# Performance work log

Hardware: AMD Instinct MI355X
Metric: run time of the kernel (lower is better)

## Reference

```python
import jax, jax.numpy as jnp
import numpy as np

D_MODEL = 768
N_HEAD = 12

def setup_inputs() -> dict:
    key = jax.random.key(0)
    ks = jax.random.split(key, 5)
    B, T, C = 2, 2048, D_MODEL
    s = 1.0 / np.sqrt(C)
    x = jax.random.normal(ks[0], (B, T, C), dtype=jnp.float32)
    W_attn = jax.random.normal(ks[1], (C, 3 * C), dtype=jnp.float32) * s
    b_attn = jnp.zeros((3 * C,), dtype=jnp.float32)
    W_proj = jax.random.normal(ks[2], (C, C), dtype=jnp.float32) * s
    b_proj = jnp.zeros((C,), dtype=jnp.float32)
    return {"x": x, "W_attn": W_attn, "b_attn": b_attn, "W_proj": W_proj, "b_proj": b_proj}

def reference(x, W_attn, b_attn, W_proj, b_proj):
    B, T, C = x.shape
    H, Dh = N_HEAD, C // N_HEAD
    qkv = x @ W_attn + b_attn  # [B,T,3C]
    q, k, v = jnp.split(qkv, 3, axis=-1)
    q = q.reshape(B, T, H, Dh).transpose(0, 2, 1, 3)  # [B,H,T,Dh]
    k = k.reshape(B, T, H, Dh).transpose(0, 2, 1, 3)
    v = v.reshape(B, T, H, Dh).transpose(0, 2, 1, 3)
    att = jnp.einsum('bhqd,bhkd->bhqk', q, k) * (1.0 / np.sqrt(Dh))
    mask = jnp.tril(jnp.ones((T, T), dtype=bool))  # causal
    att = jnp.where(mask, att, -jnp.inf)
    att = jax.nn.softmax(att, axis=-1)
    y = jnp.einsum('bhqk,bhkd->bhqd', att, v)
    y = y.transpose(0, 2, 1, 3).reshape(B, T, C)
    return y @ W_proj + b_proj
```

## Files before the change

### kernel.cpp

```cpp
#include <hip/hip_runtime.h>
#include <hip/hip_bf16.h>
#include <math.h>

#define BB 2
#define TT 2048
#define CC 768
#define HH 12
#define DD 64
#define KD 768
#define NCH 80

#define QSCALE 0.18033688011112044f
#define THR2 11.5f

typedef __attribute__((ext_vector_type(8))) short bf16x8;
typedef __attribute__((ext_vector_type(4))) float f32x4;
typedef __attribute__((ext_vector_type(4))) float f32x4v;
typedef __attribute__((ext_vector_type(4))) ushort u16x4;

static __device__ __forceinline__ ushort f2bf(float f) {
  union { float f; unsigned u; } v; v.f = f;
  unsigned r = v.u + 0x7FFF + ((v.u >> 16) & 1);
  return (ushort)(r >> 16);
}
static __device__ __forceinline__ float bf2f(ushort u) {
  union { unsigned u; float f; } v; v.u = ((unsigned)u) << 16;
  return v.f;
}

__global__ __launch_bounds__(256) void cvt_bf16(const float* __restrict__ in,
                                                ushort* __restrict__ out, int n4) {
  int i = blockIdx.x * 256 + threadIdx.x;
  if (i >= n4) return;
  f32x4v v = ((const f32x4v*)in)[i];
  u16x4 o;
  o.x = f2bf(v.x); o.y = f2bf(v.y); o.z = f2bf(v.z); o.w = f2bf(v.w);
  ((u16x4*)out)[i] = o;
}

__global__ __launch_bounds__(256) void transpose_cvt(const float* __restrict__ W,
                                                     ushort* __restrict__ Wt,
                                                     int K, int N) {
  __shared__ float t[32][33];
  const int n0 = blockIdx.x * 32, k0 = blockIdx.y * 32;
  const int tx = threadIdx.x & 31, ty = threadIdx.x >> 5;
#pragma unroll
  for (int j = 0; j < 32; j += 8)
    t[ty + j][tx] = W[(size_t)(k0 + ty + j) * N + n0 + tx];
  __syncthreads();
#pragma unroll
  for (int j = 0; j < 32; j += 8)
    Wt[(size_t)(n0 + ty + j) * K + k0 + tx] = f2bf(t[tx][ty + j]);
}

__global__ __launch_bounds__(256) void gemm_mfma(
    const ushort* __restrict__ A, const ushort* __restrict__ Bt,
    const float* __restrict__ bias, int N, int mode,
    ushort* __restrict__ Qo, ushort* __restrict__ Ko, ushort* __restrict__ Vo,
    float* __restrict__ Of) {
  __shared__ ushort As[128 * 32];
  __shared__ ushort Bs[128 * 32];
  const int tid = threadIdx.x;
  const int w = tid >> 6, lane = tid & 63;
  const int wr = w >> 1, wc = w & 1;
  const int grp = lane >> 4, colk = lane & 15;
  const int bm = blockIdx.y * 128, bn = blockIdx.x * 128;

  f32x4 acc[4][4] = {};

  auto* AsL = (__attribute__((address_space(3))) char*)As;
  auto* BsL = (__attribute__((address_space(3))) char*)Bs;

  for (int k0 = 0; k0 < KD; k0 += 32) {
#pragma unroll
    for (int i = 0; i < 2; ++i) {
      const int idx = tid + i * 256;
      const int row = idx >> 2, g = idx & 3;
      const int eoff = (g * 8) ^ ((row & 3) << 3);
      const ushort* sa = A + (size_t)(bm + row) * KD + k0 + eoff;
      const ushort* sb = Bt + (size_t)(bn + row) * KD + k0 + eoff;
      __builtin_amdgcn_global_load_lds(
          (const __attribute__((address_space(1))) void*)sa,
          (__attribute__((address_space(3))) void*)(AsL + w * 1024 + i * 4096), 16, 0, 0);
      __builtin_amdgcn_global_load_lds(
          (const __attribute__((address_space(1))) void*)sb,
          (__attribute__((address_space(3))) void*)(BsL + w * 1024 + i * 4096), 16, 0, 0);
    }
    __syncthreads();

    bf16x8 af[4], bf[4];
    const int sw = (colk & 3) << 3;
#pragma unroll
    for (int m = 0; m < 4; ++m)
      af[m] = *(const bf16x8*)&As[(wr * 64 + m * 16 + colk) * 32 + ((grp * 8) ^ sw)];
#pragma unroll
    for (int n = 0; n < 4; ++n)
      bf[n] = *(const bf16x8*)&Bs[(wc * 64 + n * 16 + colk) * 32 + ((grp * 8) ^ sw)];
#pragma unroll
    for (int m = 0; m < 4; ++m)
#pragma unroll
      for (int n = 0; n < 4; ++n)
        acc[m][n] = __builtin_amdgcn_mfma_f32_16x16x32_bf16(af[m], bf[n], acc[m][n], 0, 0, 0);
    __syncthreads();
  }

#pragma unroll
  for (int m = 0; m < 4; ++m) {
    const int gro = bm + wr * 64 + m * 16 + grp * 4;
#pragma unroll
    for (int n = 0; n < 4; ++n) {
      const int col = bn + wc * 64 + n * 16 + colk;
      const float bv = bias[col];
#pragma unroll
      for (int j = 0; j < 4; ++j) {
        const int row = gro + j;
        float v = acc[m][n][j] + bv;
        if (mode == 0) {
          const int which = col / CC;
          const int c = col - which * CC;
          const int hh = c >> 6, d = c & 63;
          const int b = row >> 11, t = row & 2047;
          if (which == 0) v *= QSCALE;
          const ushort bvv = f2bf(v);
          if (which == 0)
            Qo[((size_t)((b * HH + hh) * TT + t)) * DD + d] = bvv;
          else if (which == 1)
            Ko[((size_t)((b * HH + hh) * TT + t)) * DD + d] = bvv;
          else
            Vo[((size_t)((b * HH + hh) * DD + d)) * TT + t] = bvv;
        } else {
          Of[(size_t)row * N + col] = v;
        }
      }
    }
  }
}

__global__ __launch_bounds__(256) void attn_mfma(
    const ushort* __restrict__ Q, const ushort* __restrict__ K,
    const ushort* __restrict__ Vt, ushort* __restrict__ Po,
    float* __restrict__ Pml) {
  const int c = NCH - 1 - (int)blockIdx.x;
  int qq, ci;
  if (c < 8)       { qq = c;                              ci = 0; }
  else if (c < 24) { int o_ = c - 8;  qq = 8  + (o_ >> 1); ci = o_ & 1; }
  else if (c < 48) { int o_ = c - 24; qq = 16 + o_ / 3;    ci = o_ % 3; }
  else             { int o_ = c - 48; qq = 24 + (o_ >> 2); ci = o_ & 3; }
  const int h = blockIdx.y, b = blockIdx.z;
  const int bh = b * HH + h;
  const size_t hb = (size_t)bh * TT * DD;
  const int kbase = ci * 512;
  const int nt = min(8, qq + 1 - ci * 8);

  __shared__ ushort Ks[64][72];
  __shared__ ushort Vs[64][72];
  __shared__ ushort Ps[4][16][72];
  __shared__ float scw[4][16];

  const int tid = threadIdx.x;
  const int w = tid >> 6, lane = tid & 63;
  const int grp = lane >> 4, colk = lane & 15;
  const int q0w = qq * 64 + w * 16;
  const int qme = q0w + colk;

  const ushort* Kg = K + hb;
  const ushort* Vg = Vt + hb;

  bf16x8 qf[2];
  {
    const ushort* qp = Q + hb + (size_t)(q0w + colk) * DD + 8 * grp;
    qf[0] = *(const bf16x8*)(qp);
    qf[1] = *(const bf16x8*)(qp + 32);
  }

  f32x4 o[4] = {};
  float m = -1e30f, l = 0.f;

  const int srow = tid >> 2;
  const int scol = (tid & 3) * 16;

  {
    bf16x8 k0a = *(const bf16x8*)&Kg[(size_t)(kbase + srow) * DD + scol];
    bf16x8 k0b = *(const bf16x8*)&Kg[(size_t)(kbase + srow) * DD + scol + 8];
    bf16x8 v0a = *(const bf16x8*)&Vg[(size_t)srow * TT + kbase + scol];
    bf16x8 v0b = *(const bf16x8*)&Vg[(size_t)srow * TT + kbase + scol + 8];
    *(bf16x8*)&Ks[srow][scol] = k0a;
    *(bf16x8*)&Ks[srow][scol + 8] = k0b;
    *(bf16x8*)&Vs[srow][scol] = v0a;
    *(bf16x8*)&Vs[srow][scol + 8] = v0b;
  }
  __syncthreads();

  for (int it = 0; it < nt; ++it) {
    const int k0 = kbase + it * 64;
    const bool pfn = (it + 1 < nt);
    bf16x8 nk0, nk1, nv0, nv1;
    if (pfn) {
      nk0 = *(const bf16x8*)&Kg[(size_t)(k0 + 64 + srow) * DD + scol];
      nk1 = *(const bf16x8*)&Kg[(size_t)(k0 + 64 + srow) * DD + scol + 8];
      nv0 = *(const bf16x8*)&Vg[(size_t)srow * TT + k0 + 64 + scol];
      nv1 = *(const bf16x8*)&Vg[(size_t)srow * TT + k0 + 64 + scol + 8];
    }

    f32x4 s2[4] = {};
#pragma unroll
    for (int kb = 0; kb < 4; ++kb) {
      bf16x8 kf0 = *(const bf16x8*)&Ks[16 * kb + colk][8 * grp];
      bf16x8 kf1 = *(const bf16x8*)&Ks[16 * kb + colk][32 + 8 * grp];
      s2[kb] = __builtin_amdgcn_mfma_f32_16x16x32_bf16(kf0, qf[0], s2[kb], 0, 0, 0);
      s2[kb] = __builtin_amdgcn_mfma_f32_16x16x32_bf16(kf1, qf[1], s2[kb], 0, 0, 0);
    }

    if (k0 + 63 > q0w) {
#pragma unroll
      for (int kb = 0; kb < 4; ++kb)
#pragma unroll
        for (int r = 0; r < 4; ++r)
          if (k0 + 16 * kb + 4 * grp + r > qme) s2[kb][r] = -1e30f;
    }
    float pm = -1e30f;
#pragma unroll
    for (int kb = 0; kb < 4; ++kb)
      pm = fmaxf(pm, fmaxf(fmaxf(s2[kb][0], s2[kb][1]), fmaxf(s2[kb][2], s2[kb][3])));
    pm = fmaxf(pm, __shfl_xor(pm, 16));
    pm = fmaxf(pm, __shfl_xor(pm, 32));

    if (__any(pm > m + THR2)) {
      const float mn = fmaxf(m, pm);
      const float sc = exp2f(m - mn);
      m = mn;
      l *= sc;
      if (grp == 0) scw[w][colk] = sc;
      const f32x4 s4 = *(const f32x4*)&scw[w][4 * grp];
#pragma unroll
      for (int n = 0; n < 4; ++n)
#pragma unroll
        for (int r = 0; r < 4; ++r) o[n][r] *= s4[r];
    }

    float ps = 0.f;
#pragma unroll
    for (int kb = 0; kb < 4; ++kb) {
      const float p0 = exp2f(s2[kb][0] - m);
      const float p1 = exp2f(s2[kb][1] - m);
      const float p2 = exp2f(s2[kb][2] - m);
      const float p3 = exp2f(s2[kb][3] - m);
      ps += (p0 + p1) + (p2 + p3);
      union { __hip_bfloat162 h2[2]; uint2 u2; } pk;
      pk.h2[0] = __float22bfloat162_rn(make_float2(p0, p1));
      pk.h2[1] = __float22bfloat162_rn(make_float2(p2, p3));
      *(uint2*)&Ps[w][colk][16 * kb + 4 * grp] = pk.u2;
    }
    ps += __shfl_xor(ps, 16);
    ps += __shfl_xor(ps, 32);
    l += ps;

    bf16x8 pf0 = *(const bf16x8*)&Ps[w][colk][8 * grp];
    bf16x8 pf1 = *(const bf16x8*)&Ps[w][colk][32 + 8 * grp];
#pragma unroll
    for (int n = 0; n < 4; ++n) {
      bf16x8 vf0 = *(const bf16x8*)&Vs[16 * n + colk][8 * grp];
      bf16x8 vf1 = *(const bf16x8*)&Vs[16 * n + colk][32 + 8 * grp];
      o[n] = __builtin_amdgcn_mfma_f32_16x16x32_bf16(pf0, vf0, o[n], 0, 0, 0);
      o[n] = __builtin_amdgcn_mfma_f32_16x16x32_bf16(pf1, vf1, o[n], 0, 0, 0);
    }

    if (pfn) {
      __syncthreads();
      *(bf16x8*)&Ks[srow][scol] = nk0;
      *(bf16x8*)&Ks[srow][scol + 8] = nk1;
      *(bf16x8*)&Vs[srow][scol] = nv0;
      *(bf16x8*)&Vs[srow][scol + 8] = nv1;
      __syncthreads();
    }
  }

  const size_t pbase = ((size_t)bh * NCH + c) * 64;
#pragma unroll
  for (int r = 0; r < 4; ++r) {
    const int row = w * 16 + grp * 4 + r;
#pragma unroll
    for (int n = 0; n < 4; ++n)
      Po[(pbase + row) * 64 + 16 * n + colk] = f2bf(o[n][r]);
  }
  if (grp == 0) {
    const int row = w * 16 + colk;
    Pml[(pbase + row) * 2] = m;
    Pml[(pbase + row) * 2 + 1] = l;
  }
}

__global__ __launch_bounds__(256) void attn_merge(
    const ushort* __restrict__ Po, const float* __restrict__ Pml,
    ushort* __restrict__ Yb) {
  const int qq = blockIdx.x, h = blockIdx.y, b = blockIdx.z;
  const int bh = b * HH + h;
  const int g = qq >> 3;
  const int nch = g + 1;
  const int gb = (g == 0) ? 0 : (g == 1) ? 8 : (g == 2) ? 24 : 48;
  const int cb = gb + nch * (qq - 8 * g);

  const int tid = threadIdx.x;
  const int row = tid >> 2;
  const int d0 = (tid & 3) * 16;

  float mi[4], li[4];
  float M = -1e30f;
#pragma unroll
  for (int i = 0; i < 4; ++i) {
    if (i < nch) {
      const size_t pb = ((size_t)bh * NCH + cb + i) * 64 + row;
      mi[i] = Pml[pb * 2];
      li[i] = Pml[pb * 2 + 1];
      M = fmaxf(M, mi[i]);
    }
  }
  float acc[16] = {};
  float lt = 0.f;
#pragma unroll
  for (int i = 0; i < 4; ++i) {
    if (i < nch) {
      const float wgt = exp2f(mi[i] - M);
      lt += li[i] * wgt;
      const ushort* pp = Po + (((size_t)bh * NCH + cb + i) * 64 + row) * 64 + d0;
      bf16x8 a = *(const bf16x8*)pp;
      bf16x8 bv = *(const bf16x8*)(pp + 8);
#pragma unroll
      for (int j = 0; j < 8; ++j) {
        acc[j] += wgt * bf2f((ushort)a[j]);
        acc[8 + j] += wgt * bf2f((ushort)bv[j]);
      }
    }
  }
  const float inv = 1.0f / lt;
  const int t = qq * 64 + row;
  ushort* yp = Yb + ((size_t)(b * TT) + t) * CC + h * DD + d0;
  bf16x8 o0, o1;
#pragma unroll
  for (int j = 0; j < 8; ++j) {
    o0[j] = (short)f2bf(acc[j] * inv);
    o1[j] = (short)f2bf(acc[8 + j] * inv);
  }
  *(bf16x8*)yp = o0;
  *(bf16x8*)(yp + 8) = o1;
}

extern "C" void kernel_launch(void* const* d_in, const int* in_sizes, int n_in,
                              void* d_out, int out_size, void* d_ws, size_t ws_size,
                              hipStream_t stream) {
  const float* x      = (const float*)d_in[0];
  const float* W_attn = (const float*)d_in[1];
  const float* b_attn = (const float*)d_in[2];
  const float* W_proj = (const float*)d_in[3];
  const float* b_proj = (const float*)d_in[4];
  float* out = (float*)d_out;

  const size_t per = (size_t)BB * TT * CC;
  ushort* Q   = (ushort*)d_ws;
  ushort* K   = Q + per;
  ushort* VtT = K + per;
  ushort* Yb  = VtT + per;
  ushort* Wpt = Yb + per;
  ushort* xb  = Wpt + (size_t)CC * CC;
  ushort* Wat = xb + per;
  ushort* Po  = xb;
  float*  Pml = (float*)(Po + (size_t)BB * HH * NCH * 64 * 64);

  cvt_bf16<<<dim3((per / 4 + 255) / 256), 256, 0, stream>>>(x, xb, (int)(per / 4));
  transpose_cvt<<<dim3(3 * CC / 32, CC / 32), 256, 0, stream>>>(W_attn, Wat, CC, 3 * CC);
  transpose_cvt<<<dim3(CC / 32, CC / 32), 256, 0, stream>>>(W_proj, Wpt, CC, CC);

  gemm_mfma<<<dim3(3 * CC / 128, BB * TT / 128), 256, 0, stream>>>(
      xb, Wat, b_attn, 3 * CC, 0, Q, K, VtT, nullptr);
  attn_mfma<<<dim3(NCH, HH, BB), 256, 0, stream>>>(Q, K, VtT, Po, Pml);
  attn_merge<<<dim3(TT / 64, HH, BB), 256, 0, stream>>>(Po, Pml, Yb);
  gemm_mfma<<<dim3(CC / 128, BB * TT / 128), 256, 0, stream>>>(
      Yb, Wpt, b_proj, CC, 1, nullptr, nullptr, nullptr, out);
}
```

Measured before the change: 122.0 us.

## Double-buffer K/V shared tiles and raise wave priority around MFMA blocks

```diff
diff --git a/kernel.cpp b/kernel.cpp
--- a/kernel.cpp
+++ b/kernel.cpp
@@ -152,8 +152,8 @@
   const int kbase = ci * 512;
   const int nt = min(8, qq + 1 - ci * 8);
 
-  __shared__ ushort Ks[64][72];
-  __shared__ ushort Vs[64][72];
+  __shared__ ushort Ks[2][64][72];
+  __shared__ ushort Vs[2][64][72];
   __shared__ ushort Ps[4][16][72];
   __shared__ float scw[4][16];
 
@@ -184,13 +184,14 @@
     bf16x8 k0b = *(const bf16x8*)&Kg[(size_t)(kbase + srow) * DD + scol + 8];
     bf16x8 v0a = *(const bf16x8*)&Vg[(size_t)srow * TT + kbase + scol];
     bf16x8 v0b = *(const bf16x8*)&Vg[(size_t)srow * TT + kbase + scol + 8];
-    *(bf16x8*)&Ks[srow][scol] = k0a;
-    *(bf16x8*)&Ks[srow][scol + 8] = k0b;
-    *(bf16x8*)&Vs[srow][scol] = v0a;
-    *(bf16x8*)&Vs[srow][scol + 8] = v0b;
+    *(bf16x8*)&Ks[0][srow][scol] = k0a;
+    *(bf16x8*)&Ks[0][srow][scol + 8] = k0b;
+    *(bf16x8*)&Vs[0][srow][scol] = v0a;
+    *(bf16x8*)&Vs[0][srow][scol + 8] = v0b;
   }
   __syncthreads();
 
+  int cur = 0;
   for (int it = 0; it < nt; ++it) {
     const int k0 = kbase + it * 64;
     const bool pfn = (it + 1 < nt);
@@ -203,13 +204,15 @@
     }
 
     f32x4 s2[4] = {};
+    __builtin_amdgcn_s_setprio(1);
 #pragma unroll
     for (int kb = 0; kb < 4; ++kb) {
-      bf16x8 kf0 = *(const bf16x8*)&Ks[16 * kb + colk][8 * grp];
-      bf16x8 kf1 = *(const bf16x8*)&Ks[16 * kb + colk][32 + 8 * grp];
+      bf16x8 kf0 = *(const bf16x8*)&Ks[cur][16 * kb + colk][8 * grp];
+      bf16x8 kf1 = *(const bf16x8*)&Ks[cur][16 * kb + colk][32 + 8 * grp];
       s2[kb] = __builtin_amdgcn_mfma_f32_16x16x32_bf16(kf0, qf[0], s2[kb], 0, 0, 0);
       s2[kb] = __builtin_amdgcn_mfma_f32_16x16x32_bf16(kf1, qf[1], s2[kb], 0, 0, 0);
     }
+    __builtin_amdgcn_s_setprio(0);
 
     if (k0 + 63 > q0w) {
 #pragma unroll
@@ -257,21 +260,23 @@
 
     bf16x8 pf0 = *(const bf16x8*)&Ps[w][colk][8 * grp];
     bf16x8 pf1 = *(const bf16x8*)&Ps[w][colk][32 + 8 * grp];
+    __builtin_amdgcn_s_setprio(1);
 #pragma unroll
     for (int n = 0; n < 4; ++n) {
-      bf16x8 vf0 = *(const bf16x8*)&Vs[16 * n + colk][8 * grp];
-      bf16x8 vf1 = *(const bf16x8*)&Vs[16 * n + colk][32 + 8 * grp];
+      bf16x8 vf0 = *(const bf16x8*)&Vs[cur][16 * n + colk][8 * grp];
+      bf16x8 vf1 = *(const bf16x8*)&Vs[cur][16 * n + colk][32 + 8 * grp];
       o[n] = __builtin_amdgcn_mfma_f32_16x16x32_bf16(pf0, vf0, o[n], 0, 0, 0);
       o[n] = __builtin_amdgcn_mfma_f32_16x16x32_bf16(pf1, vf1, o[n], 0, 0, 0);
     }
+    __builtin_amdgcn_s_setprio(0);
 
     if (pfn) {
+      *(bf16x8*)&Ks[cur ^ 1][srow][scol] = nk0;
+      *(bf16x8*)&Ks[cur ^ 1][srow][scol + 8] = nk1;
+      *(bf16x8*)&Vs[cur ^ 1][srow][scol] = nv0;
+      *(bf16x8*)&Vs[cur ^ 1][srow][scol + 8] = nv1;
       __syncthreads();
-      *(bf16x8*)&Ks[srow][scol] = nk0;
-      *(bf16x8*)&Ks[srow][scol + 8] = nk1;
-      *(bf16x8*)&Vs[srow][scol] = nv0;
-      *(bf16x8*)&Vs[srow][scol + 8] = nv1;
-      __syncthreads();
+      cur ^= 1;
     }
   }
 
```

New measurement: 127.3 us. 4.4% more time.
